# Optimization experiments

Measured on AMD Instinct MI355X. Metric: run time of the kernel, lower is better.

Reference implementation:

```python
import jax, jax.numpy as jnp
import numpy as np
from math import factorial

# ---- module config (matches init_kwargs) ----
K_MAX_L = [256, 192, 128, 64]
L_MAX = len(K_MAX_L) - 1
PADDED = [2 * ((l + 1) // 2) for l in range(L_MAX + 1)]  # [0, 2, 2, 4]
N_SAMPLES = 32768

# ---- real Clebsch-Gordan coefficients (numpy, float64, done once at import) ----

def _cg_coeff(j1, m1, j2, m2, J, M):
    # Racah formula for complex-basis CG coefficient <j1 m1 j2 m2 | J M>
    if m1 + m2 != M:
        return 0.0
    pref = (2 * J + 1) * factorial(j1 + j2 - J) * factorial(j1 - j2 + J) \
        * factorial(-j1 + j2 + J) / factorial(j1 + j2 + J + 1)
    pref *= factorial(J + M) * factorial(J - M) * factorial(j1 - m1) \
        * factorial(j1 + m1) * factorial(j2 - m2) * factorial(j2 + m2)
    kmin = max(0, j2 - J - m1, j1 + m2 - J)
    kmax = min(j1 + j2 - J, j1 - m1, j2 + m2)
    s = 0.0
    for k in range(kmin, kmax + 1):
        s += (-1) ** k / (factorial(k) * factorial(j1 + j2 - J - k)
                          * factorial(j1 - m1 - k) * factorial(j2 + m2 - k)
                          * factorial(J - j2 + m1 + k) * factorial(J - j1 - m2 + k))
    return np.sqrt(pref) * s


def _cg_complex(j1, j2, J):
    cg = np.zeros((2 * j1 + 1, 2 * j2 + 1, 2 * J + 1))
    for m1 in range(-j1, j1 + 1):
        for m2 in range(-j2, j2 + 1):
            M = m1 + m2
            if abs(M) <= J:
                cg[m1 + j1, m2 + j2, M + J] = _cg_coeff(j1, m1, j2, m2, J, M)
    return cg


def _real2complex(L):
    # maps real spherical-harmonic components to complex ones (unitary)
    res = np.zeros((2 * L + 1, 2 * L + 1), dtype=np.complex128)
    isq2 = 1.0 / np.sqrt(2.0)
    for m in range(-L, L + 1):
        if m < 0:
            res[L - m, L + m] = isq2 * 1j * (-1) ** m
            res[L + m, L + m] = -isq2 * 1j
        elif m == 0:
            res[L, L] = 1.0
        else:
            res[L - m, L + m] = isq2
            res[L + m, L + m] = isq2 * (-1) ** m
    return res


def _cg_real(l1, l2, L):
    ccg = _cg_complex(l1, l2, L).astype(np.complex128)
    tmp = np.einsum('ma,nb,mnM->abM', _real2complex(l1), _real2complex(l2), ccg)
    out = np.einsum('abM,kM->abk', tmp, np.conjugate(_real2complex(L)).T)
    return np.real(out) if (l1 + l2 + L) % 2 == 0 else np.imag(out)


def _build_U(padded_l):
    half = padded_l // 2
    blocks = [_cg_real(half, half, L) for L in range(padded_l + 1)]
    U = np.concatenate(blocks, axis=2).reshape((padded_l + 1) ** 2, (padded_l + 1) ** 2)
    assert np.allclose(U @ U.T, np.eye((padded_l + 1) ** 2), atol=1e-10)
    return U

_U_DICT = {pl: jnp.asarray(_build_U(pl), dtype=jnp.float32) for pl in sorted(set(PADDED))}

# ---- forward (pure jnp) ----

def _split_bands(features):
    # band l holds channels [k_max_l[l+1]:k_max_l[l]) of all features lp<=l
    bands = []
    for l in range(L_MAX + 1):
        lo = K_MAX_L[l + 1] if l < L_MAX else 0
        hi = K_MAX_L[l]
        bands.append([features[lp][:, :, lo:hi] for lp in range(l + 1)])
    return bands


def _uncouple(feats, U, pl):
    n, w = feats[0].shape[0], feats[0].shape[-1]
    if len(feats) < pl + 1:  # pad missing top-l block with zeros (odd l case)
        feats = feats + [jnp.zeros((n, 2 * pl + 1, w), feats[0].dtype)]
    stacked = jnp.concatenate(feats, axis=1)               # (n, (pl+1)^2, w)
    unc = jnp.einsum('MN,nNw->nMw', U, stacked)
    return unc.reshape(n, pl + 1, pl + 1, w)


def _couple(x, U, pl):
    n, w = x.shape[0], x.shape[-1]
    flat = x.reshape(n, (pl + 1) ** 2, w)
    coup = jnp.einsum('NM,nNw->nMw', U, flat)              # U.T contraction
    sizes = np.cumsum([2 * L + 1 for L in range(pl + 1)])[:-1]
    return jnp.split(coup, sizes, axis=1)


def _tensor_product(f1, f2):
    b1, b2 = _split_bands(f1), _split_bands(f2)
    coupled = []
    for l in range(L_MAX + 1):
        pl = PADDED[l]
        U = _U_DICT[pl]
        u1 = _uncouple(b1[l], U, pl)                       # (n, pl+1, pl+1, w)
        u2 = _uncouple(b2[l], U, pl)
        comb = jnp.einsum('nijw,njkw->nikw', u1, u2)       # per-channel matmul
        coupled.append(_couple(comb, U, pl))
    return tuple(
        jnp.concatenate([coupled[lp][l] for lp in range(l, L_MAX + 1)], axis=-1)
        for l in range(L_MAX + 1)
    )


def setup_inputs() -> dict:
    key = jax.random.key(0)
    keys = jax.random.split(key, 8)
    out = {}
    i = 0
    for tag in ('f1', 'f2'):
        for l in range(L_MAX + 1):
            out[f'{tag}_{l}'] = jax.random.normal(
                keys[i], (N_SAMPLES, 2 * l + 1, K_MAX_L[l]), dtype=jnp.float32)
            i += 1
    return out


def reference(f1_0, f1_1, f1_2, f1_3, f2_0, f2_1, f2_2, f2_3):
    return _tensor_product([f1_0, f1_1, f1_2, f1_3], [f2_0, f2_1, f2_2, f2_3])
```

## Files before the change

kernel.cpp:

```cpp
#include <hip/hip_runtime.h>
#include <cmath>

#define NS 32768
#define OUT1_BASE (NS * 256)
#define OUT2_BASE (OUT1_BASE + NS * 576)
#define OUT3_BASE (OUT2_BASE + NS * 640)

namespace {

static double hfact(int n) { double r = 1.0; for (int i = 2; i <= n; ++i) r *= (double)i; return r; }

static double cg_coeff(int j1, int m1, int j2, int m2, int J, int M) {
    if (m1 + m2 != M) return 0.0;
    double pref = (2.0 * J + 1.0) * hfact(j1 + j2 - J) * hfact(j1 - j2 + J)
                * hfact(-j1 + j2 + J) / hfact(j1 + j2 + J + 1);
    pref *= hfact(J + M) * hfact(J - M) * hfact(j1 - m1) * hfact(j1 + m1)
          * hfact(j2 - m2) * hfact(j2 + m2);
    int kmin = 0;
    if (j2 - J - m1 > kmin) kmin = j2 - J - m1;
    if (j1 + m2 - J > kmin) kmin = j1 + m2 - J;
    int kmax = j1 + j2 - J;
    if (j1 - m1 < kmax) kmax = j1 - m1;
    if (j2 + m2 < kmax) kmax = j2 + m2;
    double s = 0.0;
    for (int k = kmin; k <= kmax; ++k) {
        double d = hfact(k) * hfact(j1 + j2 - J - k) * hfact(j1 - m1 - k)
                 * hfact(j2 + m2 - k) * hfact(J - j2 + m1 + k) * hfact(J - j1 - m2 + k);
        s += ((k & 1) ? -1.0 : 1.0) / d;
    }
    return std::sqrt(pref) * s;
}

struct C2 { double re, im; };
static inline C2 cmul(C2 a, C2 b) { return { a.re * b.re - a.im * b.im, a.re * b.im + a.im * b.re }; }
static inline C2 cadd(C2 a, C2 b) { return { a.re + b.re, a.im + b.im }; }
static inline C2 cscale(C2 a, double s) { return { a.re * s, a.im * s }; }
static inline C2 conjc(C2 a) { return { a.re, -a.im }; }

static void real2complex(int L, C2* R) {
    int D = 2 * L + 1;
    for (int i = 0; i < D * D; ++i) R[i] = { 0.0, 0.0 };
    double isq2 = 1.0 / std::sqrt(2.0);
    for (int m = -L; m <= L; ++m) {
        double sgn = (m & 1) ? -1.0 : 1.0;
        if (m < 0) {
            R[(L - m) * D + (L + m)] = { 0.0, isq2 * sgn };
            R[(L + m) * D + (L + m)] = { 0.0, -isq2 };
        } else if (m == 0) {
            R[L * D + L] = { 1.0, 0.0 };
        } else {
            R[(L - m) * D + (L + m)] = { isq2, 0.0 };
            R[(L + m) * D + (L + m)] = { isq2 * sgn, 0.0 };
        }
    }
}

static void cg_real(int l1, int l2, int L, double* out) {
    int D1 = 2 * l1 + 1, D2 = 2 * l2 + 1, DL = 2 * L + 1;
    double ccg[5 * 5 * 9];
    for (int i = 0; i < D1 * D2 * DL; ++i) ccg[i] = 0.0;
    for (int m1 = -l1; m1 <= l1; ++m1)
        for (int m2 = -l2; m2 <= l2; ++m2) {
            int M = m1 + m2;
            if (M >= -L && M <= L)
                ccg[((m1 + l1) * D2 + (m2 + l2)) * DL + (M + L)] = cg_coeff(l1, m1, l2, m2, L, M);
        }
    C2 R1[5 * 5], R2[5 * 5], RL[9 * 9];
    real2complex(l1, R1);
    real2complex(l2, R2);
    real2complex(L, RL);
    bool even = ((l1 + l2 + L) % 2) == 0;
    for (int a = 0; a < D1; ++a)
        for (int b = 0; b < D2; ++b) {
            C2 tmp[9];
            for (int M = 0; M < DL; ++M) {
                C2 s = { 0.0, 0.0 };
                for (int m = 0; m < D1; ++m)
                    for (int n = 0; n < D2; ++n) {
                        double c = ccg[(m * D2 + n) * DL + M];
                        if (c != 0.0)
                            s = cadd(s, cscale(cmul(R1[m * D1 + a], R2[n * D2 + b]), c));
                    }
                tmp[M] = s;
            }
            for (int k = 0; k < DL; ++k) {
                C2 s = { 0.0, 0.0 };
                for (int M = 0; M < DL; ++M)
                    s = cadd(s, cmul(tmp[M], conjc(RL[M * DL + k])));
                out[(a * D2 + b) * DL + k] = even ? s.re : s.im;
            }
        }
}

static void build_U(int pl, float* U) {
    int h = pl / 2, P = pl + 1, DU = P * P;
    int off = 0;
    for (int L = 0; L <= pl; ++L) {
        int DL = 2 * L + 1;
        double blk[5 * 5 * 9];
        cg_real(h, h, L, blk);
        for (int a = 0; a < P; ++a)
            for (int b = 0; b < P; ++b)
                for (int k = 0; k < DL; ++k)
                    U[(a * P + b) * DU + (off + k)] = (float)blk[(a * P + b) * DL + k];
        off += DL;
    }
}

}


struct U9Arg  { float u[81];  };
struct U25Arg { float u[625]; };

__global__ __launch_bounds__(256) void band0_kernel(
    const float* __restrict__ f1_0, const float* __restrict__ f2_0,
    float* __restrict__ out)
{
    int t = blockIdx.x * 256 + threadIdx.x;
    int n = t >> 6, c = t & 63;
    int idx = n * 256 + 192 + c;
    out[n * 256 + c] = f1_0[idx] * f2_0[idx];
}

__global__ __launch_bounds__(256) void band1_kernel(
    const float* __restrict__ f1_0, const float* __restrict__ f1_1,
    const float* __restrict__ f2_0, const float* __restrict__ f2_1,
    float* __restrict__ out, U9Arg U)
{
    int t = blockIdx.x * 256 + threadIdx.x;
    int n = t >> 6, c = t & 63;
    int ch = 128 + c;

    float x1[4], x2[4];
    x1[0] = f1_0[n * 256 + ch];
    x2[0] = f2_0[n * 256 + ch];
#pragma unroll
    for (int m = 0; m < 3; ++m) {
        x1[1 + m] = f1_1[n * 576 + m * 192 + ch];
        x2[1 + m] = f2_1[n * 576 + m * 192 + ch];
    }

    float A[9], B[9];
#pragma unroll
    for (int M = 0; M < 9; ++M) {
        float sa = 0.f, sb = 0.f;
#pragma unroll
        for (int N = 0; N < 4; ++N) { sa += U.u[M * 9 + N] * x1[N]; sb += U.u[M * 9 + N] * x2[N]; }
        A[M] = sa; B[M] = sb;
    }

    float C[9];
#pragma unroll
    for (int i = 0; i < 3; ++i)
#pragma unroll
        for (int k = 0; k < 3; ++k) {
            float s = 0.f;
#pragma unroll
            for (int j = 0; j < 3; ++j) s += A[i * 3 + j] * B[j * 3 + k];
            C[i * 3 + k] = s;
        }

    float y[4];
#pragma unroll
    for (int M = 0; M < 4; ++M) {
        float s = 0.f;
#pragma unroll
        for (int N = 0; N < 9; ++N) s += U.u[N * 9 + M] * C[N];
        y[M] = s;
    }

    out[n * 256 + 64 + c] = y[0];
#pragma unroll
    for (int m = 0; m < 3; ++m)
        out[OUT1_BASE + n * 576 + m * 192 + c] = y[1 + m];
}

__global__ __launch_bounds__(256) void band2_kernel(
    const float* __restrict__ f1_0, const float* __restrict__ f1_1, const float* __restrict__ f1_2,
    const float* __restrict__ f2_0, const float* __restrict__ f2_1, const float* __restrict__ f2_2,
    float* __restrict__ out, U9Arg U)
{
    int t = blockIdx.x * 256 + threadIdx.x;
    int n = t >> 6, c = t & 63;
    int ch = 64 + c;

    float x1[9], x2[9];
    x1[0] = f1_0[n * 256 + ch];
    x2[0] = f2_0[n * 256 + ch];
#pragma unroll
    for (int m = 0; m < 3; ++m) {
        x1[1 + m] = f1_1[n * 576 + m * 192 + ch];
        x2[1 + m] = f2_1[n * 576 + m * 192 + ch];
    }
#pragma unroll
    for (int m = 0; m < 5; ++m) {
        x1[4 + m] = f1_2[n * 640 + m * 128 + ch];
        x2[4 + m] = f2_2[n * 640 + m * 128 + ch];
    }

    float A[9], B[9];
#pragma unroll
    for (int M = 0; M < 9; ++M) {
        float sa = 0.f, sb = 0.f;
#pragma unroll
        for (int N = 0; N < 9; ++N) { sa += U.u[M * 9 + N] * x1[N]; sb += U.u[M * 9 + N] * x2[N]; }
        A[M] = sa; B[M] = sb;
    }

    float C[9];
#pragma unroll
    for (int i = 0; i < 3; ++i)
#pragma unroll
        for (int k = 0; k < 3; ++k) {
            float s = 0.f;
#pragma unroll
            for (int j = 0; j < 3; ++j) s += A[i * 3 + j] * B[j * 3 + k];
            C[i * 3 + k] = s;
        }

    float y[9];
#pragma unroll
    for (int M = 0; M < 9; ++M) {
        float s = 0.f;
#pragma unroll
        for (int N = 0; N < 9; ++N) s += U.u[N * 9 + M] * C[N];
        y[M] = s;
    }

    out[n * 256 + 128 + c] = y[0];
#pragma unroll
    for (int m = 0; m < 3; ++m)
        out[OUT1_BASE + n * 576 + m * 192 + 64 + c] = y[1 + m];
#pragma unroll
    for (int m = 0; m < 5; ++m)
        out[OUT2_BASE + n * 640 + m * 128 + c] = y[4 + m];
}

__global__ __launch_bounds__(256) void band3_kernel(
    const float* __restrict__ f1_0, const float* __restrict__ f1_1,
    const float* __restrict__ f1_2, const float* __restrict__ f1_3,
    const float* __restrict__ f2_0, const float* __restrict__ f2_1,
    const float* __restrict__ f2_2, const float* __restrict__ f2_3,
    float* __restrict__ out, U25Arg U)
{
    int t = blockIdx.x * 256 + threadIdx.x;
    int n = t >> 6, c = t & 63;

    float x1[16], x2[16];
    x1[0] = f1_0[n * 256 + c];
    x2[0] = f2_0[n * 256 + c];
#pragma unroll
    for (int m = 0; m < 3; ++m) {
        x1[1 + m] = f1_1[n * 576 + m * 192 + c];
        x2[1 + m] = f2_1[n * 576 + m * 192 + c];
    }
#pragma unroll
    for (int m = 0; m < 5; ++m) {
        x1[4 + m] = f1_2[n * 640 + m * 128 + c];
        x2[4 + m] = f2_2[n * 640 + m * 128 + c];
    }
#pragma unroll
    for (int m = 0; m < 7; ++m) {
        x1[9 + m] = f1_3[n * 448 + m * 64 + c];
        x2[9 + m] = f2_3[n * 448 + m * 64 + c];
    }

    float A[25], B[25];
#pragma unroll
    for (int M = 0; M < 25; ++M) {
        float sa = 0.f, sb = 0.f;
#pragma unroll
        for (int N = 0; N < 16; ++N) { sa += U.u[M * 25 + N] * x1[N]; sb += U.u[M * 25 + N] * x2[N]; }
        A[M] = sa; B[M] = sb;
    }

    float C[25];
#pragma unroll
    for (int i = 0; i < 5; ++i)
#pragma unroll
        for (int k = 0; k < 5; ++k) {
            float s = 0.f;
#pragma unroll
            for (int j = 0; j < 5; ++j) s += A[i * 5 + j] * B[j * 5 + k];
            C[i * 5 + k] = s;
        }

    float y[16];
#pragma unroll
    for (int M = 0; M < 16; ++M) {
        float s = 0.f;
#pragma unroll
        for (int N = 0; N < 25; ++N) s += U.u[N * 25 + M] * C[N];
        y[M] = s;
    }

    out[n * 256 + 192 + c] = y[0];
#pragma unroll
    for (int m = 0; m < 3; ++m)
        out[OUT1_BASE + n * 576 + m * 192 + 128 + c] = y[1 + m];
#pragma unroll
    for (int m = 0; m < 5; ++m)
        out[OUT2_BASE + n * 640 + m * 128 + 64 + c] = y[4 + m];
#pragma unroll
    for (int m = 0; m < 7; ++m)
        out[OUT3_BASE + n * 448 + m * 64 + c] = y[9 + m];
}

extern "C" void kernel_launch(void* const* d_in, const int* in_sizes, int n_in,
                              void* d_out, int out_size, void* d_ws, size_t ws_size,
                              hipStream_t stream)
{
    U9Arg U9;
    U25Arg U25;
    build_U(2, U9.u);
    build_U(4, U25.u);

    const float* f1_0 = (const float*)d_in[0];
    const float* f1_1 = (const float*)d_in[1];
    const float* f1_2 = (const float*)d_in[2];
    const float* f1_3 = (const float*)d_in[3];
    const float* f2_0 = (const float*)d_in[4];
    const float* f2_1 = (const float*)d_in[5];
    const float* f2_2 = (const float*)d_in[6];
    const float* f2_3 = (const float*)d_in[7];
    float* out = (float*)d_out;

    dim3 blk(256);
    dim3 grid(NS / 4);

    band0_kernel<<<grid, blk, 0, stream>>>(f1_0, f2_0, out);
    band1_kernel<<<grid, blk, 0, stream>>>(f1_0, f1_1, f2_0, f2_1, out, U9);
    band2_kernel<<<grid, blk, 0, stream>>>(f1_0, f1_1, f1_2, f2_0, f2_1, f2_2, out, U9);
    band3_kernel<<<grid, blk, 0, stream>>>(f1_0, f1_1, f1_2, f1_3, f2_0, f2_1, f2_2, f2_3, out, U25);
}
```

Measured before the change: 166.7 us.

## Fuse four band kernels into one and bake CG coefficients as constexpr

Merges the four per-band launches into a single kernel, so each thread handles all bands for its sample and channel lane. The Clebsch-Gordan coupling matrices are now computed at compile time as constexpr tables, which removes host-side construction on every launch. Multiplies by zero coefficients are pruned at compile time through constant-folded branches. The fused kernel has higher register pressure, which may lower occupancy.

```diff
diff --git a/kernel.cpp b/kernel.cpp
--- a/kernel.cpp
+++ b/kernel.cpp
@@ -1,16 +1,22 @@
 #include <hip/hip_runtime.h>
-#include <cmath>
 
 #define NS 32768
 #define OUT1_BASE (NS * 256)
 #define OUT2_BASE (OUT1_BASE + NS * 576)
 #define OUT3_BASE (OUT2_BASE + NS * 640)
 
-namespace {
-
-static double hfact(int n) { double r = 1.0; for (int i = 2; i <= n; ++i) r *= (double)i; return r; }
-
-static double cg_coeff(int j1, int m1, int j2, int m2, int J, int M) {
+namespace cgc {
+
+constexpr double hfact(int n) { double r = 1.0; for (int i = 2; i <= n; ++i) r *= (double)i; return r; }
+
+constexpr double csqrt(double a) {
+    if (a <= 0.0) return 0.0;
+    double x = a > 1.0 ? a : 1.0;
+    for (int i = 0; i < 64; ++i) x = 0.5 * (x + a / x);
+    return x;
+}
+
+constexpr double cg_coeff(int j1, int m1, int j2, int m2, int J, int M) {
     if (m1 + m2 != M) return 0.0;
     double pref = (2.0 * J + 1.0) * hfact(j1 + j2 - J) * hfact(j1 - j2 + J)
                 * hfact(-j1 + j2 + J) / hfact(j1 + j2 + J + 1);
@@ -28,294 +34,307 @@
                  * hfact(j2 + m2 - k) * hfact(J - j2 + m1 + k) * hfact(J - j1 - m2 + k);
         s += ((k & 1) ? -1.0 : 1.0) / d;
     }
-    return std::sqrt(pref) * s;
-}
-
-struct C2 { double re, im; };
-static inline C2 cmul(C2 a, C2 b) { return { a.re * b.re - a.im * b.im, a.re * b.im + a.im * b.re }; }
-static inline C2 cadd(C2 a, C2 b) { return { a.re + b.re, a.im + b.im }; }
-static inline C2 cscale(C2 a, double s) { return { a.re * s, a.im * s }; }
-static inline C2 conjc(C2 a) { return { a.re, -a.im }; }
-
-static void real2complex(int L, C2* R) {
+    return csqrt(pref) * s;
+}
+
+struct C2 { double re; double im; };
+constexpr C2 cmul(C2 a, C2 b) { return { a.re * b.re - a.im * b.im, a.re * b.im + a.im * b.re }; }
+constexpr C2 cadd(C2 a, C2 b) { return { a.re + b.re, a.im + b.im }; }
+constexpr C2 cscale(C2 a, double s) { return { a.re * s, a.im * s }; }
+constexpr C2 conjc(C2 a) { return { a.re, -a.im }; }
+
+struct R2C { C2 r[81]; };
+
+constexpr R2C real2complex(int L) {
+    R2C R{};
     int D = 2 * L + 1;
-    for (int i = 0; i < D * D; ++i) R[i] = { 0.0, 0.0 };
-    double isq2 = 1.0 / std::sqrt(2.0);
+    double isq2 = 0.70710678118654752440084436210485;
+    isq2 = 1.0 / csqrt(2.0);
     for (int m = -L; m <= L; ++m) {
         double sgn = (m & 1) ? -1.0 : 1.0;
         if (m < 0) {
-            R[(L - m) * D + (L + m)] = { 0.0, isq2 * sgn };
-            R[(L + m) * D + (L + m)] = { 0.0, -isq2 };
+            R.r[(L - m) * D + (L + m)] = { 0.0, isq2 * sgn };
+            R.r[(L + m) * D + (L + m)] = { 0.0, -isq2 };
         } else if (m == 0) {
-            R[L * D + L] = { 1.0, 0.0 };
+            R.r[L * D + L] = { 1.0, 0.0 };
         } else {
-            R[(L - m) * D + (L + m)] = { isq2, 0.0 };
-            R[(L + m) * D + (L + m)] = { isq2 * sgn, 0.0 };
-        }
-    }
-}
-
-static void cg_real(int l1, int l2, int L, double* out) {
+            R.r[(L - m) * D + (L + m)] = { isq2, 0.0 };
+            R.r[(L + m) * D + (L + m)] = { isq2 * sgn, 0.0 };
+        }
+    }
+    return R;
+}
+
+struct Blk { double v[225]; };
+
+constexpr Blk cg_real(int l1, int l2, int L) {
+    Blk out{};
     int D1 = 2 * l1 + 1, D2 = 2 * l2 + 1, DL = 2 * L + 1;
-    double ccg[5 * 5 * 9];
-    for (int i = 0; i < D1 * D2 * DL; ++i) ccg[i] = 0.0;
+    double ccg[225] = {};
     for (int m1 = -l1; m1 <= l1; ++m1)
         for (int m2 = -l2; m2 <= l2; ++m2) {
             int M = m1 + m2;
             if (M >= -L && M <= L)
                 ccg[((m1 + l1) * D2 + (m2 + l2)) * DL + (M + L)] = cg_coeff(l1, m1, l2, m2, L, M);
         }
-    C2 R1[5 * 5], R2[5 * 5], RL[9 * 9];
-    real2complex(l1, R1);
-    real2complex(l2, R2);
-    real2complex(L, RL);
+    R2C R1 = real2complex(l1);
+    R2C R2 = real2complex(l2);
+    R2C RL = real2complex(L);
     bool even = ((l1 + l2 + L) % 2) == 0;
     for (int a = 0; a < D1; ++a)
         for (int b = 0; b < D2; ++b) {
-            C2 tmp[9];
+            C2 tmp[9] = {};
             for (int M = 0; M < DL; ++M) {
                 C2 s = { 0.0, 0.0 };
                 for (int m = 0; m < D1; ++m)
-                    for (int n = 0; n < D2; ++n) {
-                        double c = ccg[(m * D2 + n) * DL + M];
-                        if (c != 0.0)
-                            s = cadd(s, cscale(cmul(R1[m * D1 + a], R2[n * D2 + b]), c));
+                    for (int nn = 0; nn < D2; ++nn) {
+                        double cc = ccg[(m * D2 + nn) * DL + M];
+                        if (cc != 0.0)
+                            s = cadd(s, cscale(cmul(R1.r[m * D1 + a], R2.r[nn * D2 + b]), cc));
                     }
                 tmp[M] = s;
             }
             for (int k = 0; k < DL; ++k) {
                 C2 s = { 0.0, 0.0 };
                 for (int M = 0; M < DL; ++M)
-                    s = cadd(s, cmul(tmp[M], conjc(RL[M * DL + k])));
-                out[(a * D2 + b) * DL + k] = even ? s.re : s.im;
-            }
-        }
-}
-
-static void build_U(int pl, float* U) {
-    int h = pl / 2, P = pl + 1, DU = P * P;
+                    s = cadd(s, cmul(tmp[M], conjc(RL.r[M * DL + k])));
+                out.v[(a * D2 + b) * DL + k] = even ? s.re : s.im;
+            }
+        }
+    return out;
+}
+
+constexpr Blk B2_0 = cg_real(1, 1, 0);
+constexpr Blk B2_1 = cg_real(1, 1, 1);
+constexpr Blk B2_2 = cg_real(1, 1, 2);
+constexpr Blk B4_0 = cg_real(2, 2, 0);
+constexpr Blk B4_1 = cg_real(2, 2, 1);
+constexpr Blk B4_2 = cg_real(2, 2, 2);
+constexpr Blk B4_3 = cg_real(2, 2, 3);
+constexpr Blk B4_4 = cg_real(2, 2, 4);
+
+struct U9T  { float u[81];  };
+struct U25T { float u[625]; };
+
+constexpr U9T build_U9() {
+    U9T U{};
+    const Blk* bl[3] = { &B2_0, &B2_1, &B2_2 };
     int off = 0;
-    for (int L = 0; L <= pl; ++L) {
+    for (int L = 0; L <= 2; ++L) {
         int DL = 2 * L + 1;
-        double blk[5 * 5 * 9];
-        cg_real(h, h, L, blk);
-        for (int a = 0; a < P; ++a)
-            for (int b = 0; b < P; ++b)
+        for (int a = 0; a < 3; ++a)
+            for (int b = 0; b < 3; ++b)
                 for (int k = 0; k < DL; ++k)
-                    U[(a * P + b) * DU + (off + k)] = (float)blk[(a * P + b) * DL + k];
+                    U.u[(a * 3 + b) * 9 + (off + k)] = (float)bl[L]->v[(a * 3 + b) * DL + k];
         off += DL;
     }
-}
-
-}
-
-
-struct U9Arg  { float u[81];  };
-struct U25Arg { float u[625]; };
-
-__global__ __launch_bounds__(256) void band0_kernel(
-    const float* __restrict__ f1_0, const float* __restrict__ f2_0,
-    float* __restrict__ out)
-{
-    int t = blockIdx.x * 256 + threadIdx.x;
-    int n = t >> 6, c = t & 63;
-    int idx = n * 256 + 192 + c;
-    out[n * 256 + c] = f1_0[idx] * f2_0[idx];
-}
-
-__global__ __launch_bounds__(256) void band1_kernel(
-    const float* __restrict__ f1_0, const float* __restrict__ f1_1,
-    const float* __restrict__ f2_0, const float* __restrict__ f2_1,
-    float* __restrict__ out, U9Arg U)
-{
-    int t = blockIdx.x * 256 + threadIdx.x;
-    int n = t >> 6, c = t & 63;
-    int ch = 128 + c;
-
-    float x1[4], x2[4];
-    x1[0] = f1_0[n * 256 + ch];
-    x2[0] = f2_0[n * 256 + ch];
-#pragma unroll
-    for (int m = 0; m < 3; ++m) {
-        x1[1 + m] = f1_1[n * 576 + m * 192 + ch];
-        x2[1 + m] = f2_1[n * 576 + m * 192 + ch];
-    }
-
-    float A[9], B[9];
-#pragma unroll
-    for (int M = 0; M < 9; ++M) {
-        float sa = 0.f, sb = 0.f;
-#pragma unroll
-        for (int N = 0; N < 4; ++N) { sa += U.u[M * 9 + N] * x1[N]; sb += U.u[M * 9 + N] * x2[N]; }
-        A[M] = sa; B[M] = sb;
-    }
-
-    float C[9];
-#pragma unroll
-    for (int i = 0; i < 3; ++i)
-#pragma unroll
-        for (int k = 0; k < 3; ++k) {
-            float s = 0.f;
-#pragma unroll
-            for (int j = 0; j < 3; ++j) s += A[i * 3 + j] * B[j * 3 + k];
-            C[i * 3 + k] = s;
-        }
-
-    float y[4];
-#pragma unroll
-    for (int M = 0; M < 4; ++M) {
-        float s = 0.f;
-#pragma unroll
-        for (int N = 0; N < 9; ++N) s += U.u[N * 9 + M] * C[N];
-        y[M] = s;
-    }
-
-    out[n * 256 + 64 + c] = y[0];
-#pragma unroll
-    for (int m = 0; m < 3; ++m)
-        out[OUT1_BASE + n * 576 + m * 192 + c] = y[1 + m];
-}
-
-__global__ __launch_bounds__(256) void band2_kernel(
-    const float* __restrict__ f1_0, const float* __restrict__ f1_1, const float* __restrict__ f1_2,
-    const float* __restrict__ f2_0, const float* __restrict__ f2_1, const float* __restrict__ f2_2,
-    float* __restrict__ out, U9Arg U)
-{
-    int t = blockIdx.x * 256 + threadIdx.x;
-    int n = t >> 6, c = t & 63;
-    int ch = 64 + c;
-
-    float x1[9], x2[9];
-    x1[0] = f1_0[n * 256 + ch];
-    x2[0] = f2_0[n * 256 + ch];
-#pragma unroll
-    for (int m = 0; m < 3; ++m) {
-        x1[1 + m] = f1_1[n * 576 + m * 192 + ch];
-        x2[1 + m] = f2_1[n * 576 + m * 192 + ch];
-    }
-#pragma unroll
-    for (int m = 0; m < 5; ++m) {
-        x1[4 + m] = f1_2[n * 640 + m * 128 + ch];
-        x2[4 + m] = f2_2[n * 640 + m * 128 + ch];
-    }
-
-    float A[9], B[9];
-#pragma unroll
-    for (int M = 0; M < 9; ++M) {
-        float sa = 0.f, sb = 0.f;
-#pragma unroll
-        for (int N = 0; N < 9; ++N) { sa += U.u[M * 9 + N] * x1[N]; sb += U.u[M * 9 + N] * x2[N]; }
-        A[M] = sa; B[M] = sb;
-    }
-
-    float C[9];
-#pragma unroll
-    for (int i = 0; i < 3; ++i)
-#pragma unroll
-        for (int k = 0; k < 3; ++k) {
-            float s = 0.f;
-#pragma unroll
-            for (int j = 0; j < 3; ++j) s += A[i * 3 + j] * B[j * 3 + k];
-            C[i * 3 + k] = s;
-        }
-
-    float y[9];
-#pragma unroll
-    for (int M = 0; M < 9; ++M) {
-        float s = 0.f;
-#pragma unroll
-        for (int N = 0; N < 9; ++N) s += U.u[N * 9 + M] * C[N];
-        y[M] = s;
-    }
-
-    out[n * 256 + 128 + c] = y[0];
-#pragma unroll
-    for (int m = 0; m < 3; ++m)
-        out[OUT1_BASE + n * 576 + m * 192 + 64 + c] = y[1 + m];
-#pragma unroll
-    for (int m = 0; m < 5; ++m)
-        out[OUT2_BASE + n * 640 + m * 128 + c] = y[4 + m];
-}
-
-__global__ __launch_bounds__(256) void band3_kernel(
+    return U;
+}
+
+constexpr U25T build_U25() {
+    U25T U{};
+    const Blk* bl[5] = { &B4_0, &B4_1, &B4_2, &B4_3, &B4_4 };
+    int off = 0;
+    for (int L = 0; L <= 4; ++L) {
+        int DL = 2 * L + 1;
+        for (int a = 0; a < 5; ++a)
+            for (int b = 0; b < 5; ++b)
+                for (int k = 0; k < DL; ++k)
+                    U.u[(a * 5 + b) * 25 + (off + k)] = (float)bl[L]->v[(a * 5 + b) * DL + k];
+        off += DL;
+    }
+    return U;
+}
+
+constexpr U9T  U9c  = build_U9();
+constexpr U25T U25c = build_U25();
+
+}
+
+
+__global__ __launch_bounds__(256) void tp_fused_kernel(
     const float* __restrict__ f1_0, const float* __restrict__ f1_1,
     const float* __restrict__ f1_2, const float* __restrict__ f1_3,
     const float* __restrict__ f2_0, const float* __restrict__ f2_1,
     const float* __restrict__ f2_2, const float* __restrict__ f2_3,
-    float* __restrict__ out, U25Arg U)
+    float* __restrict__ out)
 {
-    int t = blockIdx.x * 256 + threadIdx.x;
-    int n = t >> 6, c = t & 63;
-
-    float x1[16], x2[16];
-    x1[0] = f1_0[n * 256 + c];
-    x2[0] = f2_0[n * 256 + c];
-#pragma unroll
-    for (int m = 0; m < 3; ++m) {
-        x1[1 + m] = f1_1[n * 576 + m * 192 + c];
-        x2[1 + m] = f2_1[n * 576 + m * 192 + c];
-    }
-#pragma unroll
-    for (int m = 0; m < 5; ++m) {
-        x1[4 + m] = f1_2[n * 640 + m * 128 + c];
-        x2[4 + m] = f2_2[n * 640 + m * 128 + c];
-    }
-#pragma unroll
-    for (int m = 0; m < 7; ++m) {
-        x1[9 + m] = f1_3[n * 448 + m * 64 + c];
-        x2[9 + m] = f2_3[n * 448 + m * 64 + c];
-    }
-
-    float A[25], B[25];
-#pragma unroll
-    for (int M = 0; M < 25; ++M) {
-        float sa = 0.f, sb = 0.f;
-#pragma unroll
-        for (int N = 0; N < 16; ++N) { sa += U.u[M * 25 + N] * x1[N]; sb += U.u[M * 25 + N] * x2[N]; }
-        A[M] = sa; B[M] = sb;
-    }
-
-    float C[25];
-#pragma unroll
-    for (int i = 0; i < 5; ++i)
-#pragma unroll
-        for (int k = 0; k < 5; ++k) {
+    using namespace cgc;
+    const int t = blockIdx.x * 256 + threadIdx.x;
+    const int n = t >> 6, c = t & 63;
+    const int r0 = n * 256, r1 = n * 576, r2 = n * 640, r3 = n * 448;
+
+    out[r0 + c] = f1_0[r0 + 192 + c] * f2_0[r0 + 192 + c];
+
+    {
+        const int ch = 128 + c;
+        float x1[4], x2[4];
+        x1[0] = f1_0[r0 + ch];
+        x2[0] = f2_0[r0 + ch];
+#pragma unroll
+        for (int m = 0; m < 3; ++m) {
+            x1[1 + m] = f1_1[r1 + m * 192 + ch];
+            x2[1 + m] = f2_1[r1 + m * 192 + ch];
+        }
+        float A[9], B[9];
+#pragma unroll
+        for (int M = 0; M < 9; ++M) {
+            float sa = 0.f, sb = 0.f;
+#pragma unroll
+            for (int N = 0; N < 4; ++N)
+                if (U9c.u[M * 9 + N] != 0.0f) {
+                    sa += U9c.u[M * 9 + N] * x1[N];
+                    sb += U9c.u[M * 9 + N] * x2[N];
+                }
+            A[M] = sa; B[M] = sb;
+        }
+        float C[9];
+#pragma unroll
+        for (int i = 0; i < 3; ++i)
+#pragma unroll
+            for (int k = 0; k < 3; ++k) {
+                float s = 0.f;
+#pragma unroll
+                for (int j = 0; j < 3; ++j) s += A[i * 3 + j] * B[j * 3 + k];
+                C[i * 3 + k] = s;
+            }
+        float y[4];
+#pragma unroll
+        for (int M = 0; M < 4; ++M) {
             float s = 0.f;
 #pragma unroll
-            for (int j = 0; j < 5; ++j) s += A[i * 5 + j] * B[j * 5 + k];
-            C[i * 5 + k] = s;
-        }
-
-    float y[16];
-#pragma unroll
-    for (int M = 0; M < 16; ++M) {
-        float s = 0.f;
-#pragma unroll
-        for (int N = 0; N < 25; ++N) s += U.u[N * 25 + M] * C[N];
-        y[M] = s;
-    }
-
-    out[n * 256 + 192 + c] = y[0];
-#pragma unroll
-    for (int m = 0; m < 3; ++m)
-        out[OUT1_BASE + n * 576 + m * 192 + 128 + c] = y[1 + m];
-#pragma unroll
-    for (int m = 0; m < 5; ++m)
-        out[OUT2_BASE + n * 640 + m * 128 + 64 + c] = y[4 + m];
-#pragma unroll
-    for (int m = 0; m < 7; ++m)
-        out[OUT3_BASE + n * 448 + m * 64 + c] = y[9 + m];
+            for (int N = 0; N < 9; ++N)
+                if (U9c.u[N * 9 + M] != 0.0f) s += U9c.u[N * 9 + M] * C[N];
+            y[M] = s;
+        }
+        out[r0 + 64 + c] = y[0];
+#pragma unroll
+        for (int m = 0; m < 3; ++m)
+            out[OUT1_BASE + r1 + m * 192 + c] = y[1 + m];
+    }
+
+    {
+        const int ch = 64 + c;
+        float x1[9], x2[9];
+        x1[0] = f1_0[r0 + ch];
+        x2[0] = f2_0[r0 + ch];
+#pragma unroll
+        for (int m = 0; m < 3; ++m) {
+            x1[1 + m] = f1_1[r1 + m * 192 + ch];
+            x2[1 + m] = f2_1[r1 + m * 192 + ch];
+        }
+#pragma unroll
+        for (int m = 0; m < 5; ++m) {
+            x1[4 + m] = f1_2[r2 + m * 128 + ch];
+            x2[4 + m] = f2_2[r2 + m * 128 + ch];
+        }
+        float A[9], B[9];
+#pragma unroll
+        for (int M = 0; M < 9; ++M) {
+            float sa = 0.f, sb = 0.f;
+#pragma unroll
+            for (int N = 0; N < 9; ++N)
+                if (U9c.u[M * 9 + N] != 0.0f) {
+                    sa += U9c.u[M * 9 + N] * x1[N];
+                    sb += U9c.u[M * 9 + N] * x2[N];
+                }
+            A[M] = sa; B[M] = sb;
+        }
+        float C[9];
+#pragma unroll
+        for (int i = 0; i < 3; ++i)
+#pragma unroll
+            for (int k = 0; k < 3; ++k) {
+                float s = 0.f;
+#pragma unroll
+                for (int j = 0; j < 3; ++j) s += A[i * 3 + j] * B[j * 3 + k];
+                C[i * 3 + k] = s;
+            }
+        float y[9];
+#pragma unroll
+        for (int M = 0; M < 9; ++M) {
+            float s = 0.f;
+#pragma unroll
+            for (int N = 0; N < 9; ++N)
+                if (U9c.u[N * 9 + M] != 0.0f) s += U9c.u[N * 9 + M] * C[N];
+            y[M] = s;
+        }
+        out[r0 + 128 + c] = y[0];
+#pragma unroll
+        for (int m = 0; m < 3; ++m)
+            out[OUT1_BASE + r1 + m * 192 + 64 + c] = y[1 + m];
+#pragma unroll
+        for (int m = 0; m < 5; ++m)
+            out[OUT2_BASE + r2 + m * 128 + c] = y[4 + m];
+    }
+
+    {
+        float x1[16], x2[16];
+        x1[0] = f1_0[r0 + c];
+        x2[0] = f2_0[r0 + c];
+#pragma unroll
+        for (int m = 0; m < 3; ++m) {
+            x1[1 + m] = f1_1[r1 + m * 192 + c];
+            x2[1 + m] = f2_1[r1 + m * 192 + c];
+        }
+#pragma unroll
+        for (int m = 0; m < 5; ++m) {
+            x1[4 + m] = f1_2[r2 + m * 128 + c];
+            x2[4 + m] = f2_2[r2 + m * 128 + c];
+        }
+#pragma unroll
+        for (int m = 0; m < 7; ++m) {
+            x1[9 + m] = f1_3[r3 + m * 64 + c];
+            x2[9 + m] = f2_3[r3 + m * 64 + c];
+        }
+        float A[25], B[25];
+#pragma unroll
+        for (int M = 0; M < 25; ++M) {
+            float sa = 0.f, sb = 0.f;
+#pragma unroll
+            for (int N = 0; N < 16; ++N)
+                if (U25c.u[M * 25 + N] != 0.0f) {
+                    sa += U25c.u[M * 25 + N] * x1[N];
+                    sb += U25c.u[M * 25 + N] * x2[N];
+                }
+            A[M] = sa; B[M] = sb;
+        }
+        float C[25];
+#pragma unroll
+        for (int i = 0; i < 5; ++i)
+#pragma unroll
+            for (int k = 0; k < 5; ++k) {
+                float s = 0.f;
+#pragma unroll
+                for (int j = 0; j < 5; ++j) s += A[i * 5 + j] * B[j * 5 + k];
+                C[i * 5 + k] = s;
+            }
+        float y[16];
+#pragma unroll
+        for (int M = 0; M < 16; ++M) {
+            float s = 0.f;
+#pragma unroll
+            for (int N = 0; N < 25; ++N)
+                if (U25c.u[N * 25 + M] != 0.0f) s += U25c.u[N * 25 + M] * C[N];
+            y[M] = s;
+        }
+        out[r0 + 192 + c] = y[0];
+#pragma unroll
+        for (int m = 0; m < 3; ++m)
+            out[OUT1_BASE + r1 + m * 192 + 128 + c] = y[1 + m];
+#pragma unroll
+        for (int m = 0; m < 5; ++m)
+            out[OUT2_BASE + r2 + m * 128 + 64 + c] = y[4 + m];
+#pragma unroll
+        for (int m = 0; m < 7; ++m)
+            out[OUT3_BASE + r3 + m * 64 + c] = y[9 + m];
+    }
 }
 
 extern "C" void kernel_launch(void* const* d_in, const int* in_sizes, int n_in,
                               void* d_out, int out_size, void* d_ws, size_t ws_size,
                               hipStream_t stream)
 {
-    U9Arg U9;
-    U25Arg U25;
-    build_U(2, U9.u);
-    build_U(4, U25.u);
-
     const float* f1_0 = (const float*)d_in[0];
     const float* f1_1 = (const float*)d_in[1];
     const float* f1_2 = (const float*)d_in[2];
@@ -329,8 +348,6 @@
     dim3 blk(256);
     dim3 grid(NS / 4);
 
-    band0_kernel<<<grid, blk, 0, stream>>>(f1_0, f2_0, out);
-    band1_kernel<<<grid, blk, 0, stream>>>(f1_0, f1_1, f2_0, f2_1, out, U9);
-    band2_kernel<<<grid, blk, 0, stream>>>(f1_0, f1_1, f1_2, f2_0, f2_1, f2_2, out, U9);
-    band3_kernel<<<grid, blk, 0, stream>>>(f1_0, f1_1, f1_2, f1_3, f2_0, f2_1, f2_2, f2_3, out, U25);
-}
+    tp_fused_kernel<<<grid, blk, 0, stream>>>(f1_0, f1_1, f1_2, f1_3,
+                                              f2_0, f2_1, f2_2, f2_3, out);
+}
```

Measured after the change: 143.0 us. 1.17x faster.
